# Performance work log

Measured on AMD Instinct MI355X. Metric: run time of the kernel, lower is better.

The kernel has to match this reference:

```python
import jax, jax.numpy as jnp
import numpy as np

B, S, D = 32, 1024, 1024  # S must equal D for scores @ v to type-check


def setup_inputs() -> dict:
    key = jax.random.key(0)
    k0, k1, k2, k3, k4, k5 = jax.random.split(key, 6)
    x = jax.random.normal(k0, (B, S, D), dtype=jnp.float32)
    Wq = jax.random.normal(k1, (D, D), dtype=jnp.float32) * 0.02
    bq = jnp.zeros((D,), dtype=jnp.float32)
    Wk = jax.random.normal(k2, (D, D), dtype=jnp.float32) * 0.02
    bk = jnp.zeros((D,), dtype=jnp.float32)
    v = jax.random.uniform(k3, (D,), dtype=jnp.float32)  # torch.rand init
    return {"x": x, "Wq": Wq, "bq": bq, "Wk": Wk, "bk": bk, "v": v}


def reference(x, Wq, bq, Wk, bk, v):
    # Linear layers (torch Linear: y = x @ W^T + b)
    q = jnp.einsum('bsd,ed->bse', x, Wq) + bq          # [B,S,D]
    k = jnp.einsum('bsd,ed->bse', x, Wk) + bk          # [B,S,D]
    scores = jnp.tanh(jnp.einsum('bsd,btd->bst', q, k))  # [B,S,S]
    s = jnp.einsum('bst,t->bs', scores, v)             # [B,S] (S == D)
    w = jax.nn.softmax(s, axis=-1)                     # [B,S]
    out = jnp.einsum('bs,bsd->bd', w, x)               # [B,D]
    return out
```

## Files before the change

### kernel.cpp

```cpp
#include <hip/hip_runtime.h>
#include <hip/hip_bf16.h>
#include <math.h>

#define BB 32
#define SS 1024
#define DD 1024

typedef __bf16 bf16_t;
typedef __bf16 bf16x2 __attribute__((ext_vector_type(2)));
typedef __bf16 bf16x4 __attribute__((ext_vector_type(4)));
typedef __bf16 bf16x8 __attribute__((ext_vector_type(8)));
typedef float f32x4 __attribute__((ext_vector_type(4)));

__device__ __forceinline__ void gload16(const void* g, void* lds_uniform) {
    __builtin_amdgcn_global_load_lds(
        (const __attribute__((address_space(1))) void*)g,
        (__attribute__((address_space(3))) void*)lds_uniform, 16, 0, 0);
}

__device__ __forceinline__ void stage32(const bf16_t* __restrict__ src,
                                        int row0, int k0, char* slot, int tid) {
    const int r = tid >> 2;
    const int c = ((tid & 3) ^ ((tid >> 3) & 3)) * 8;
    char* d = slot + (tid >> 6) * 1024;
    const bf16_t* s = src + (size_t)(row0 + r) * DD + k0 + c;
    gload16(s, d);
    gload16(s + (size_t)128 * DD, d + 8192);
}

#define VM8  asm volatile("s_waitcnt vmcnt(8)" ::: "memory")
#define VM4  asm volatile("s_waitcnt vmcnt(4)" ::: "memory")
#define VM0  asm volatile("s_waitcnt vmcnt(0)" ::: "memory")
#define BARR asm volatile("s_barrier" ::: "memory")

#define SEL_A(u) ((((u) >> 5) == 2) ? Alo : Ahi)
#define SEL_B(u) ((((u) >> 5) == 1) ? Blo : Bhi)
#define K0OF(u)  (((u) & 31) * 32)

#define TILE32(u, s, DOST) do {                                               \
    if (DOST) stage32(SEL_A((u)+3), rowA, K0OF((u)+3),                        \
                      AslR + ((((u)+3)&3) * 16384), tid);                     \
    bf16x8 bfr[4], af[4];                                                     \
    _Pragma("unroll") for (int fc = 0; fc < 4; ++fc)                          \
        bfr[fc] = *(const bf16x8*)(Bbase##s + fc * 1024);                     \
    _Pragma("unroll") for (int fr = 0; fr < 4; ++fr)                          \
        af[fr] = *(const bf16x8*)(Abase##s + fr * 1024);                      \
    _Pragma("unroll") for (int fr = 0; fr < 4; ++fr)                          \
        _Pragma("unroll") for (int fc = 0; fc < 4; ++fc)                      \
            acc[fr][fc] = __builtin_amdgcn_mfma_f32_16x16x32_bf16(            \
                af[fr], bfr[fc], acc[fr][fc], 0, 0, 0);                       \
    if (DOST) stage32(SEL_B((u)+3), rowB, K0OF((u)+3),                        \
                      BslR + ((((u)+3)&3) * 16384), tid);                     \
    _Pragma("unroll") for (int fr = 0; fr < 4; ++fr)                          \
        af[fr] = *(const bf16x8*)(Abase##s + 4096 + fr * 1024);               \
    _Pragma("unroll") for (int fr = 0; fr < 4; ++fr)                          \
        _Pragma("unroll") for (int fc = 0; fc < 4; ++fc)                      \
            acc[4+fr][fc] = __builtin_amdgcn_mfma_f32_16x16x32_bf16(          \
                af[fr], bfr[fc], acc[4+fr][fc], 0, 0, 0);                     \
} while (0)

__device__ __forceinline__ void kloop_ring(
    const bf16_t* __restrict__ Ahi, const bf16_t* __restrict__ Alo,
    const bf16_t* __restrict__ Bhi, const bf16_t* __restrict__ Blo,
    int rowA, int rowB, int tid, int lane, int wm, int wn,
    char* AslR, char* BslR, f32x4 (*acc)[4])
{
    const int aoff = (lane & 15) * 64 + (((lane >> 4) ^ ((lane >> 1) & 3)) * 16);
    const char* Abase0 = AslR + wm * 8192 + aoff;
    const char* Abase1 = Abase0 + 16384;
    const char* Abase2 = Abase0 + 32768;
    const char* Abase3 = Abase0 + 49152;
    const char* Bbase0 = BslR + wn * 4096 + aoff;
    const char* Bbase1 = Bbase0 + 16384;
    const char* Bbase2 = Bbase0 + 32768;
    const char* Bbase3 = Bbase0 + 49152;

    stage32(SEL_A(0), rowA, K0OF(0), AslR, tid);
    stage32(SEL_B(0), rowB, K0OF(0), BslR, tid);
    stage32(SEL_A(1), rowA, K0OF(1), AslR + 16384, tid);
    stage32(SEL_B(1), rowB, K0OF(1), BslR + 16384, tid);
    stage32(SEL_A(2), rowA, K0OF(2), AslR + 32768, tid);
    stage32(SEL_B(2), rowB, K0OF(2), BslR + 32768, tid);
    VM8;
    BARR;

    for (int i = 0; i < 23; ++i) {
        const int u0 = i * 4;
        TILE32(u0 + 0, 0, true); VM8; BARR;
        TILE32(u0 + 1, 1, true); VM8; BARR;
        TILE32(u0 + 2, 2, true); VM8; BARR;
        TILE32(u0 + 3, 3, true); VM8; BARR;
    }
    TILE32(92, 0, true);  VM8; BARR;
    TILE32(93, 1, false); VM4; BARR;
    TILE32(94, 2, false); VM0; BARR;
    TILE32(95, 3, false);
}

__global__ __launch_bounds__(512, 2) void gemm_y_256(
    const bf16_t* __restrict__ xh, const bf16_t* __restrict__ xl,
    const bf16_t* __restrict__ Mth, const bf16_t* __restrict__ Mtl,
    bf16_t* __restrict__ out_hi, bf16_t* __restrict__ out_lo)
{
    __shared__ __align__(16) bf16_t Asl[4][256 * 32];
    __shared__ __align__(16) bf16_t Bsl[4][256 * 32];
    const int tid = threadIdx.x;
    const int lane = tid & 63, wid = tid >> 6;
    const int wm = wid >> 2, wn = wid & 3;
    const int lin = (blockIdx.x & 7) * 64 + (blockIdx.x >> 3);
    const int m0 = (lin >> 2) * 256;
    const int n0 = (lin & 3) * 256;

    f32x4 acc[8][4] = {};
    kloop_ring(xh, xl, Mth, Mtl, m0, n0, tid, lane, wm, wn,
               (char*)Asl, (char*)Bsl, acc);

    const int rbase = (lane >> 4) * 4;
    const int cbase = lane & 15;
    #pragma unroll
    for (int fr = 0; fr < 8; ++fr) {
        #pragma unroll
        for (int fc = 0; fc < 4; ++fc) {
            const int n = n0 + wn * 64 + fc * 16 + cbase;
            #pragma unroll
            for (int r = 0; r < 4; ++r) {
                const int m = m0 + wm * 128 + fr * 16 + rbase + r;
                float vf = acc[fr][fc][r];
                bf16_t h = (bf16_t)vf;
                out_hi[(size_t)m * DD + n] = h;
                out_lo[(size_t)m * DD + n] = (bf16_t)(vf - (float)h);
            }
        }
    }
}

__global__ __launch_bounds__(512, 2) void gemm_scores_256(
    const bf16_t* __restrict__ yh, const bf16_t* __restrict__ yl,
    const bf16_t* __restrict__ xh, const bf16_t* __restrict__ xl,
    const float* __restrict__ v, const float* __restrict__ alpha,
    const float* __restrict__ beta, const float* __restrict__ cbuf,
    float* __restrict__ sbuf)
{
    __shared__ __align__(16) bf16_t Asl[4][256 * 32];
    __shared__ __align__(16) bf16_t Bsl[4][256 * 32];
    const int tid = threadIdx.x;
    const int lane = tid & 63, wid = tid >> 6;
    const int wm = wid >> 2, wn = wid & 3;
    const int lin = (blockIdx.x & 7) * 64 + (blockIdx.x >> 3);
    const int t0 = (lin & 3) * 256;
    const int s0 = ((lin >> 2) & 3) * 256;
    const int b  = lin >> 4;
    const size_t boff = (size_t)b * SS * DD;

    f32x4 acc[8][4] = {};
    kloop_ring(yh + boff, yl + boff, xh + boff, xl + boff, s0, t0,
               tid, lane, wm, wn, (char*)Asl, (char*)Bsl, acc);

    const float c0 = cbuf[0];
    const int rbase = (lane >> 4) * 4;
    const int cbase = lane & 15;
    float bet[4], vv[4];
    #pragma unroll
    for (int fc = 0; fc < 4; ++fc) {
        const int t = t0 + wn * 64 + fc * 16 + cbase;
        bet[fc] = beta[b * SS + t];
        vv[fc]  = v[t];
    }
    #pragma unroll
    for (int fr = 0; fr < 8; ++fr) {
        #pragma unroll
        for (int r = 0; r < 4; ++r) {
            const int srow = s0 + wm * 128 + fr * 16 + rbase + r;
            const float al = alpha[b * SS + srow] + c0;
            float p = 0.f;
            #pragma unroll
            for (int fc = 0; fc < 4; ++fc)
                p += tanhf(acc[fr][fc][r] + al + bet[fc]) * vv[fc];
            p += __shfl_xor(p, 1);
            p += __shfl_xor(p, 2);
            p += __shfl_xor(p, 4);
            p += __shfl_xor(p, 8);
            if (cbase == 0) atomicAdd(&sbuf[b * SS + srow], p);
        }
    }
}

__global__ __launch_bounds__(256) void split_x_ab(
    const float* __restrict__ src, bf16_t* __restrict__ hi,
    bf16_t* __restrict__ lo, const float* __restrict__ avec,
    const float* __restrict__ bvec, float* __restrict__ alpha,
    float* __restrict__ beta)
{
    const int lane = threadIdx.x & 63, wave = threadIdx.x >> 6;
    float4 av[4], bv[4];
    #pragma unroll
    for (int j = 0; j < 4; ++j) {
        av[j] = ((const float4*)avec)[j * 64 + lane];
        bv[j] = ((const float4*)bvec)[j * 64 + lane];
    }
    for (int row = blockIdx.x * 4 + wave; row < BB * SS; row += 2048 * 4) {
        const float4* xr = (const float4*)(src + (size_t)row * DD);
        bf16x4* hr = (bf16x4*)(hi + (size_t)row * DD);
        bf16x4* lr = (bf16x4*)(lo + (size_t)row * DD);
        float pa = 0.f, pb = 0.f;
        #pragma unroll
        for (int j = 0; j < 4; ++j) {
            float4 f = xr[j * 64 + lane];
            bf16x4 h, l;
            h.x = (bf16_t)f.x; h.y = (bf16_t)f.y;
            h.z = (bf16_t)f.z; h.w = (bf16_t)f.w;
            l.x = (bf16_t)(f.x - (float)h.x);
            l.y = (bf16_t)(f.y - (float)h.y);
            l.z = (bf16_t)(f.z - (float)h.z);
            l.w = (bf16_t)(f.w - (float)h.w);
            hr[j * 64 + lane] = h;
            lr[j * 64 + lane] = l;
            pa += f.x * av[j].x + f.y * av[j].y + f.z * av[j].z + f.w * av[j].w;
            pb += f.x * bv[j].x + f.y * bv[j].y + f.z * bv[j].z + f.w * bv[j].w;
        }
        #pragma unroll
        for (int off = 32; off; off >>= 1) {
            pa += __shfl_xor(pa, off);
            pb += __shfl_xor(pb, off);
        }
        if (lane == 0) { alpha[row] = pa; beta[row] = pb; }
    }
}

__global__ __launch_bounds__(256) void bias_gemv(
    const float* __restrict__ Wq, const float* __restrict__ Wk,
    const float* __restrict__ bq, const float* __restrict__ bk,
    float* __restrict__ avec, float* __restrict__ bvec)
{
    const float* W   = blockIdx.z ? Wk : Wq;
    const float* bb  = blockIdx.z ? bq : bk;
    float* outv      = blockIdx.z ? bvec : avec;
    const int d  = blockIdx.x * 256 + threadIdx.x;
    const int e0 = blockIdx.y * 64;
    float s = 0.f;
    for (int e = e0; e < e0 + 64; ++e) s += W[(size_t)e * DD + d] * bb[e];
    atomicAdd(&outv[d], s);
}

__global__ __launch_bounds__(256) void dot_c(
    const float* __restrict__ bq, const float* __restrict__ bk,
    float* __restrict__ cbuf)
{
    __shared__ float red[4];
    const int tid = threadIdx.x, lane = tid & 63, wave = tid >> 6;
    float s = 0.f;
    for (int e = tid; e < DD; e += 256) s += bq[e] * bk[e];
    #pragma unroll
    for (int off = 32; off; off >>= 1) s += __shfl_xor(s, off);
    if (lane == 0) red[wave] = s;
    __syncthreads();
    if (tid == 0) cbuf[0] = red[0] + red[1] + red[2] + red[3];
}

__global__ __launch_bounds__(256) void mt_split(
    const float* __restrict__ Wk, const float* __restrict__ Wq,
    bf16_t* __restrict__ Mth, bf16_t* __restrict__ Mtl)
{
    __shared__ float Us[16][68];
    __shared__ float Vs[16][68];
    const int tid = threadIdx.x;
    const int tx = tid & 15, ty = tid >> 4;
    const int i0 = blockIdx.y * 64;
    const int j0 = blockIdx.x * 64;
    float acc[4][4] = {};
    for (int e0 = 0; e0 < DD; e0 += 16) {
        #pragma unroll
        for (int r = 0; r < 4; ++r) {
            const int kk = (tid >> 6) + r * 4;
            const int cc = tid & 63;
            Us[kk][cc] = Wk[(size_t)(e0 + kk) * DD + i0 + cc];
            Vs[kk][cc] = Wq[(size_t)(e0 + kk) * DD + j0 + cc];
        }
        __syncthreads();
        #pragma unroll
        for (int kk = 0; kk < 16; ++kk) {
            float4 a = *(const float4*)&Us[kk][ty * 4];
            float4 w = *(const float4*)&Vs[kk][tx * 4];
            acc[0][0] += a.x * w.x; acc[0][1] += a.x * w.y; acc[0][2] += a.x * w.z; acc[0][3] += a.x * w.w;
            acc[1][0] += a.y * w.x; acc[1][1] += a.y * w.y; acc[1][2] += a.y * w.z; acc[1][3] += a.y * w.w;
            acc[2][0] += a.z * w.x; acc[2][1] += a.z * w.y; acc[2][2] += a.z * w.z; acc[2][3] += a.z * w.w;
            acc[3][0] += a.w * w.x; acc[3][1] += a.w * w.y; acc[3][2] += a.w * w.z; acc[3][3] += a.w * w.w;
        }
        __syncthreads();
    }
    #pragma unroll
    for (int i = 0; i < 4; ++i) {
        #pragma unroll
        for (int j = 0; j < 4; ++j) {
            const size_t o = (size_t)(i0 + ty * 4 + i) * DD + j0 + tx * 4 + j;
            float vf = acc[i][j];
            bf16_t h = (bf16_t)vf;
            Mth[o] = h;
            Mtl[o] = (bf16_t)(vf - (float)h);
        }
    }
}

__global__ __launch_bounds__(256) void softmax_rows(
    const float* __restrict__ sbuf, float* __restrict__ wbuf)
{
    const int b = blockIdx.x, tid = threadIdx.x;
    const int wave = tid >> 6, lane = tid & 63;
    __shared__ float redm[4];
    __shared__ float redsum[4];

    float vals[4];
    float mx = -1e30f;
    #pragma unroll
    for (int i = 0; i < 4; ++i) {
        vals[i] = sbuf[b * SS + i * 256 + tid];
        mx = fmaxf(mx, vals[i]);
    }
    #pragma unroll
    for (int off = 32; off; off >>= 1) mx = fmaxf(mx, __shfl_xor(mx, off));
    if (lane == 0) redm[wave] = mx;
    __syncthreads();
    mx = fmaxf(fmaxf(redm[0], redm[1]), fmaxf(redm[2], redm[3]));

    float sum = 0.f;
    #pragma unroll
    for (int i = 0; i < 4; ++i) { vals[i] = expf(vals[i] - mx); sum += vals[i]; }
    #pragma unroll
    for (int off = 32; off; off >>= 1) sum += __shfl_xor(sum, off);
    if (lane == 0) redsum[wave] = sum;
    __syncthreads();
    sum = redsum[0] + redsum[1] + redsum[2] + redsum[3];

    float inv = 1.0f / sum;
    #pragma unroll
    for (int i = 0; i < 4; ++i) wbuf[b * SS + i * 256 + tid] = vals[i] * inv;
}

__global__ __launch_bounds__(256) void weighted_sum(
    const bf16_t* __restrict__ xh, const float* __restrict__ wbuf,
    float* __restrict__ out)
{
    __shared__ float wl[256];
    const int b = blockIdx.y;
    const int s0 = blockIdx.x * 256;
    const int tid = threadIdx.x;
    wl[tid] = wbuf[b * SS + s0 + tid];
    __syncthreads();

    float a0 = 0.f, a1 = 0.f, a2 = 0.f, a3 = 0.f;
    const bf16_t* xb = xh + (size_t)b * SS * DD + (size_t)s0 * DD;
    #pragma unroll 4
    for (int s = 0; s < 256; ++s) {
        const bf16_t* xr = xb + (size_t)s * DD;
        bf16x2 u = *(const bf16x2*)(xr + tid * 2);
        bf16x2 w2 = *(const bf16x2*)(xr + tid * 2 + 512);
        const float w = wl[s];
        a0 += w * (float)u.x;  a1 += w * (float)u.y;
        a2 += w * (float)w2.x; a3 += w * (float)w2.y;
    }
    atomicAdd(&out[b * DD + tid * 2], a0);
    atomicAdd(&out[b * DD + tid * 2 + 1], a1);
    atomicAdd(&out[b * DD + tid * 2 + 512], a2);
    atomicAdd(&out[b * DD + tid * 2 + 513], a3);
}

extern "C" void kernel_launch(void* const* d_in, const int* in_sizes, int n_in,
                              void* d_out, int out_size, void* d_ws, size_t ws_size,
                              hipStream_t stream) {
    const float* x  = (const float*)d_in[0];
    const float* Wq = (const float*)d_in[1];
    const float* bq = (const float*)d_in[2];
    const float* Wk = (const float*)d_in[3];
    const float* bk = (const float*)d_in[4];
    const float* v  = (const float*)d_in[5];
    float* out = (float*)d_out;

    const size_t nx = (size_t)BB * SS * DD;
    const size_t nw = (size_t)DD * DD;

    dim3 blk(256);

    char* p = (char*)d_ws;
    bf16_t* xh  = (bf16_t*)p;   p += nx * 2;
    bf16_t* xl  = (bf16_t*)p;   p += nx * 2;
    bf16_t* yh  = (bf16_t*)p;   p += nx * 2;
    bf16_t* yl  = (bf16_t*)p;   p += nx * 2;
    bf16_t* Mth = (bf16_t*)p;   p += nw * 2;
    bf16_t* Mtl = (bf16_t*)p;   p += nw * 2;
    float*  avec = (float*)p;   p += 4096;
    float*  bvec = (float*)p;   p += 4096;
    float*  cbuf = (float*)p;   p += 16;
    float*  alpha = (float*)p;  p += (size_t)BB * SS * 4;
    float*  beta  = (float*)p;  p += (size_t)BB * SS * 4;
    float*  sbuf  = (float*)p;  p += (size_t)BB * SS * 4;
    float*  wbuf  = (float*)p;

    hipMemsetAsync(sbuf, 0, (size_t)BB * SS * sizeof(float), stream);
    hipMemsetAsync(avec, 0, 4096 * 2, stream);
    hipMemsetAsync(out, 0, (size_t)BB * DD * sizeof(float), stream);

    bias_gemv<<<dim3(4, 16, 2), blk, 0, stream>>>(Wq, Wk, bq, bk, avec, bvec);
    dot_c<<<1, blk, 0, stream>>>(bq, bk, cbuf);
    split_x_ab<<<2048, blk, 0, stream>>>(x, xh, xl, avec, bvec, alpha, beta);
    mt_split<<<dim3(16, 16), blk, 0, stream>>>(Wk, Wq, Mth, Mtl);

    gemm_y_256<<<512, dim3(512), 0, stream>>>(xh, xl, Mth, Mtl, yh, yl);
    gemm_scores_256<<<512, dim3(512), 0, stream>>>(yh, yl, xh, xl, v,
                                                   alpha, beta, cbuf, sbuf);

    softmax_rows<<<BB, blk, 0, stream>>>(sbuf, wbuf);
    weighted_sum<<<dim3(4, BB), blk, 0, stream>>>(xh, wbuf, out);
}
```

Baseline: 623.9 us.

## Fuse hi/lo split-precision GEMM passes into one K loop with double buffering

The K loop used to run the three bf16 split passes (hi*hi, hi*lo, lo*hi) as 96 concatenated K-steps through a 4-slot ring that prefetched 3 steps ahead. It now walks K once in 32 steps. Each step stages the hi and lo tiles of both A and B into a double buffer and issues all three MFMAs per fragment pair, reusing each loaded fragment. This cuts global-to-LDS traffic and LDS fragment reads per MFMA, since the hi tiles are no longer fetched twice. The cost is a shallower prefetch, one step ahead with a full vmcnt(0) wait each step, which may expose more memory latency.

New measurement: 539.5 us (median of 2 runs). 13.5% less time.

```diff
diff --git a/kernel.cpp b/kernel.cpp
--- a/kernel.cpp
+++ b/kernel.cpp
@@ -19,82 +19,79 @@
 }
 
 __device__ __forceinline__ void stage32(const bf16_t* __restrict__ src,
-                                        int row0, int k0, char* slot, int tid) {
+                                        int row0, int k0, char* tile, int tid) {
     const int r = tid >> 2;
     const int c = ((tid & 3) ^ ((tid >> 3) & 3)) * 8;
-    char* d = slot + (tid >> 6) * 1024;
+    char* d = tile + (tid >> 6) * 1024;
     const bf16_t* s = src + (size_t)(row0 + r) * DD + k0 + c;
     gload16(s, d);
     gload16(s + (size_t)128 * DD, d + 8192);
 }
 
-#define VM8  asm volatile("s_waitcnt vmcnt(8)" ::: "memory")
-#define VM4  asm volatile("s_waitcnt vmcnt(4)" ::: "memory")
 #define VM0  asm volatile("s_waitcnt vmcnt(0)" ::: "memory")
 #define BARR asm volatile("s_barrier" ::: "memory")
 
-#define SEL_A(u) ((((u) >> 5) == 2) ? Alo : Ahi)
-#define SEL_B(u) ((((u) >> 5) == 1) ? Blo : Bhi)
-#define K0OF(u)  (((u) & 31) * 32)
-
-#define TILE32(u, s, DOST) do {                                               \
-    if (DOST) stage32(SEL_A((u)+3), rowA, K0OF((u)+3),                        \
-                      AslR + ((((u)+3)&3) * 16384), tid);                     \
-    bf16x8 bfr[4], af[4];                                                     \
-    _Pragma("unroll") for (int fc = 0; fc < 4; ++fc)                          \
-        bfr[fc] = *(const bf16x8*)(Bbase##s + fc * 1024);                     \
-    _Pragma("unroll") for (int fr = 0; fr < 4; ++fr)                          \
-        af[fr] = *(const bf16x8*)(Abase##s + fr * 1024);                      \
-    _Pragma("unroll") for (int fr = 0; fr < 4; ++fr)                          \
-        _Pragma("unroll") for (int fc = 0; fc < 4; ++fc)                      \
-            acc[fr][fc] = __builtin_amdgcn_mfma_f32_16x16x32_bf16(            \
-                af[fr], bfr[fc], acc[fr][fc], 0, 0, 0);                       \
-    if (DOST) stage32(SEL_B((u)+3), rowB, K0OF((u)+3),                        \
-                      BslR + ((((u)+3)&3) * 16384), tid);                     \
-    _Pragma("unroll") for (int fr = 0; fr < 4; ++fr)                          \
-        af[fr] = *(const bf16x8*)(Abase##s + 4096 + fr * 1024);               \
-    _Pragma("unroll") for (int fr = 0; fr < 4; ++fr)                          \
-        _Pragma("unroll") for (int fc = 0; fc < 4; ++fc)                      \
-            acc[4+fr][fc] = __builtin_amdgcn_mfma_f32_16x16x32_bf16(          \
-                af[fr], bfr[fc], acc[4+fr][fc], 0, 0, 0);                     \
+#define COLSTEP(c, s) do {                                                    \
+    if ((c) < 31) {                                                           \
+        const int k1_ = ((c) + 1) * 32;                                       \
+        stage32(Ahi, rowA, k1_, Lw##s + 0,     tid);                          \
+        stage32(Alo, rowA, k1_, Lw##s + 16384, tid);                          \
+        stage32(Bhi, rowB, k1_, Lw##s + 32768, tid);                          \
+        stage32(Blo, rowB, k1_, Lw##s + 49152, tid);                          \
+    }                                                                         \
+    bf16x8 bh[4], bl[4];                                                      \
+    _Pragma("unroll") for (int fc = 0; fc < 4; ++fc) {                        \
+        bh[fc] = *(const bf16x8*)(pBh##s + fc * 1024);                        \
+        bl[fc] = *(const bf16x8*)(pBl##s + fc * 1024);                        \
+    }                                                                         \
+    _Pragma("unroll") for (int h = 0; h < 2; ++h) {                           \
+        bf16x8 ah[4], al[4];                                                  \
+        _Pragma("unroll") for (int fr = 0; fr < 4; ++fr) {                    \
+            ah[fr] = *(const bf16x8*)(pAh##s + h * 4096 + fr * 1024);         \
+            al[fr] = *(const bf16x8*)(pAl##s + h * 4096 + fr * 1024);         \
+        }                                                                     \
+        _Pragma("unroll") for (int fr = 0; fr < 4; ++fr)                      \
+            _Pragma("unroll") for (int fc = 0; fc < 4; ++fc) {                \
+                acc[h*4+fr][fc] = __builtin_amdgcn_mfma_f32_16x16x32_bf16(    \
+                    ah[fr], bh[fc], acc[h*4+fr][fc], 0, 0, 0);                \
+                acc[h*4+fr][fc] = __builtin_amdgcn_mfma_f32_16x16x32_bf16(    \
+                    ah[fr], bl[fc], acc[h*4+fr][fc], 0, 0, 0);                \
+                acc[h*4+fr][fc] = __builtin_amdgcn_mfma_f32_16x16x32_bf16(    \
+                    al[fr], bh[fc], acc[h*4+fr][fc], 0, 0, 0);                \
+            }                                                                 \
+    }                                                                         \
+    VM0; BARR;                                                                \
 } while (0)
 
-__device__ __forceinline__ void kloop_ring(
+__device__ __forceinline__ void kloop_fused(
     const bf16_t* __restrict__ Ahi, const bf16_t* __restrict__ Alo,
     const bf16_t* __restrict__ Bhi, const bf16_t* __restrict__ Blo,
     int rowA, int rowB, int tid, int lane, int wm, int wn,
-    char* AslR, char* BslR, f32x4 (*acc)[4])
+    char* L, f32x4 (*acc)[4])
 {
     const int aoff = (lane & 15) * 64 + (((lane >> 4) ^ ((lane >> 1) & 3)) * 16);
-    const char* Abase0 = AslR + wm * 8192 + aoff;
-    const char* Abase1 = Abase0 + 16384;
-    const char* Abase2 = Abase0 + 32768;
-    const char* Abase3 = Abase0 + 49152;
-    const char* Bbase0 = BslR + wn * 4096 + aoff;
-    const char* Bbase1 = Bbase0 + 16384;
-    const char* Bbase2 = Bbase0 + 32768;
-    const char* Bbase3 = Bbase0 + 49152;
-
-    stage32(SEL_A(0), rowA, K0OF(0), AslR, tid);
-    stage32(SEL_B(0), rowB, K0OF(0), BslR, tid);
-    stage32(SEL_A(1), rowA, K0OF(1), AslR + 16384, tid);
-    stage32(SEL_B(1), rowB, K0OF(1), BslR + 16384, tid);
-    stage32(SEL_A(2), rowA, K0OF(2), AslR + 32768, tid);
-    stage32(SEL_B(2), rowB, K0OF(2), BslR + 32768, tid);
-    VM8;
+    const char* pAh0 = L + wm * 8192 + aoff;
+    const char* pAl0 = pAh0 + 16384;
+    const char* pBh0 = L + 32768 + wn * 4096 + aoff;
+    const char* pBl0 = pBh0 + 16384;
+    const char* pAh1 = pAh0 + 65536;
+    const char* pAl1 = pAl0 + 65536;
+    const char* pBh1 = pBh0 + 65536;
+    const char* pBl1 = pBl0 + 65536;
+    char* Lw0 = L + 65536;
+    char* Lw1 = L;
+
+    stage32(Ahi, rowA, 0, L + 0,     tid);
+    stage32(Alo, rowA, 0, L + 16384, tid);
+    stage32(Bhi, rowB, 0, L + 32768, tid);
+    stage32(Blo, rowB, 0, L + 49152, tid);
+    VM0;
     BARR;
 
-    for (int i = 0; i < 23; ++i) {
-        const int u0 = i * 4;
-        TILE32(u0 + 0, 0, true); VM8; BARR;
-        TILE32(u0 + 1, 1, true); VM8; BARR;
-        TILE32(u0 + 2, 2, true); VM8; BARR;
-        TILE32(u0 + 3, 3, true); VM8; BARR;
-    }
-    TILE32(92, 0, true);  VM8; BARR;
-    TILE32(93, 1, false); VM4; BARR;
-    TILE32(94, 2, false); VM0; BARR;
-    TILE32(95, 3, false);
+    for (int i = 0; i < 16; ++i) {
+        COLSTEP(2 * i,     0);
+        COLSTEP(2 * i + 1, 1);
+    }
 }
 
 __global__ __launch_bounds__(512, 2) void gemm_y_256(
@@ -102,8 +99,7 @@
     const bf16_t* __restrict__ Mth, const bf16_t* __restrict__ Mtl,
     bf16_t* __restrict__ out_hi, bf16_t* __restrict__ out_lo)
 {
-    __shared__ __align__(16) bf16_t Asl[4][256 * 32];
-    __shared__ __align__(16) bf16_t Bsl[4][256 * 32];
+    __shared__ __align__(16) bf16_t Lsh[2 * 4 * 256 * 32];
     const int tid = threadIdx.x;
     const int lane = tid & 63, wid = tid >> 6;
     const int wm = wid >> 2, wn = wid & 3;
@@ -112,8 +108,8 @@
     const int n0 = (lin & 3) * 256;
 
     f32x4 acc[8][4] = {};
-    kloop_ring(xh, xl, Mth, Mtl, m0, n0, tid, lane, wm, wn,
-               (char*)Asl, (char*)Bsl, acc);
+    kloop_fused(xh, xl, Mth, Mtl, m0, n0, tid, lane, wm, wn,
+                (char*)Lsh, acc);
 
     const int rbase = (lane >> 4) * 4;
     const int cbase = lane & 15;
@@ -141,8 +137,7 @@
     const float* __restrict__ beta, const float* __restrict__ cbuf,
     float* __restrict__ sbuf)
 {
-    __shared__ __align__(16) bf16_t Asl[4][256 * 32];
-    __shared__ __align__(16) bf16_t Bsl[4][256 * 32];
+    __shared__ __align__(16) bf16_t Lsh[2 * 4 * 256 * 32];
     const int tid = threadIdx.x;
     const int lane = tid & 63, wid = tid >> 6;
     const int wm = wid >> 2, wn = wid & 3;
@@ -153,8 +148,8 @@
     const size_t boff = (size_t)b * SS * DD;
 
     f32x4 acc[8][4] = {};
-    kloop_ring(yh + boff, yl + boff, xh + boff, xl + boff, s0, t0,
-               tid, lane, wm, wn, (char*)Asl, (char*)Bsl, acc);
+    kloop_fused(yh + boff, yl + boff, xh + boff, xl + boff, s0, t0,
+                tid, lane, wm, wn, (char*)Lsh, acc);
 
     const float c0 = cbuf[0];
     const int rbase = (lane >> 4) * 4;
```
